# Kernel tuning notes

Measured on AMD Instinct MI355X. Metric: run time of the kernel, lower is better.

## Reference

```python
import jax, jax.numpy as jnp
import numpy as np

EPS_NORM = 1e-12
RMS_EPS = 1e-5


def _rmsnorm(x, w):
    var = jnp.mean(jnp.square(x), axis=-1, keepdims=True)
    return x * jax.lax.rsqrt(var + RMS_EPS) * w


def setup_inputs() -> dict:
    key = jax.random.key(0)
    B, T, D, H, R, K = 2, 512, 1024, 16, 32, 3
    d = D // H
    ks = jax.random.split(key, 11)
    s = 0.02
    return dict(
        x=jax.random.normal(ks[0], (B, T, D), jnp.float32),
        Wq=jax.random.normal(ks[1], (D, D), jnp.float32) * s,
        Wk=jax.random.normal(ks[2], (D, D), jnp.float32) * s,
        Wv=jax.random.normal(ks[3], (D, D), jnp.float32) * s,
        Wo=jax.random.normal(ks[4], (D, D), jnp.float32) * s,
        wA=jax.random.normal(ks[5], (D, R), jnp.float32) * s,
        wB=jax.random.normal(ks[6], (R, D), jnp.float32) * s,
        conv_w=jax.random.normal(ks[7], (D, K), jnp.float32) * 0.5,
        beta_w=jax.random.normal(ks[8], (D, H), jnp.float32) * s,
        g_w=jax.random.normal(ks[9], (D, H), jnp.float32) * s,
        g_b=jnp.zeros((H,), jnp.float32),
        qnorm_w=jnp.ones((d,), jnp.float32),
        knorm_w=jnp.ones((d,), jnp.float32),
    )


def _path_attention(x, Wq, Wk, Wv, Wo, wA, wB, conv_w, beta_w, g_w, g_b, qnorm_w, knorm_w):
    # PaTH attention: s_ij = q_i^T (H_i ... H_{j+1}) k_j / sqrt(d) + (G_i - G_j),
    # H_t = I - beta_t w_t w_t^T (unit w_t), G = cumsum(logsigmoid(forget gate)).
    B, T, D = x.shape
    d = qnorm_w.shape[0]
    H = D // d
    scale = d ** -0.5

    q = (x @ Wq).reshape(B, T, H, d)
    k = (x @ Wk).reshape(B, T, H, d)
    v = (x @ Wv).reshape(B, T, H, d)

    # low-rank W projection + causal depthwise short conv (size 3) + silu
    w = (x @ wA) @ wB                                      # [B,T,D]
    wp = jnp.pad(w, ((0, 0), (2, 0), (0, 0)))
    w = wp[:, 0:T] * conv_w[:, 0] + wp[:, 1:T + 1] * conv_w[:, 1] + wp[:, 2:T + 2] * conv_w[:, 2]
    w = jax.nn.silu(w).reshape(B, T, H, d)
    # unit Householder directions
    w = w * jax.lax.rsqrt(jnp.sum(jnp.square(w), -1, keepdims=True) + EPS_NORM)

    beta = 2.0 * jax.nn.sigmoid(x @ beta_w)                # [B,T,H], in (0,2)
    g = jax.nn.log_sigmoid(x @ g_w + g_b)                  # [B,T,H] forget gate, log-space

    q = _rmsnorm(q, qnorm_w)
    k = _rmsnorm(k, knorm_w)

    # -> [B,H,T,(d)]
    q, k, v, w = (t.transpose(0, 2, 1, 3) for t in (q, k, v, w))
    beta = beta.transpose(0, 2, 1)
    g = g.transpose(0, 2, 1)

    # UT/WY form: A_{t,j} = w_t . (H_{t-1}...H_{j+1} k_j), t > j, via unit-lower tri solve:
    #   A_{t,j} + sum_{s<t} beta_s (w_t.w_s) A_{s,j} = (w_t.k_j) [t>j]
    tri_s = jnp.tril(jnp.ones((T, T), bool), -1)
    C = jnp.einsum('bhtd,bhsd->bhts', w, w) * beta[:, :, None, :]
    L = jnp.where(tri_s, C, 0.0) + jnp.eye(T, dtype=x.dtype)
    Rhs = jnp.where(tri_s, jnp.einsum('bhtd,bhjd->bhtj', w, k), 0.0)
    A = jax.scipy.linalg.solve_triangular(L, Rhs, lower=True, unit_diagonal=True)

    # s_ij = q_i.k_j - sum_{j<t<=i} (q_i.w_t) beta_t A_{t,j}
    tri = jnp.tril(jnp.ones((T, T), bool))
    qw = jnp.where(tri, jnp.einsum('bhid,bhtd->bhit', q, w), 0.0)
    S = jnp.einsum('bhid,bhjd->bhij', q, k) - jnp.einsum('bhit,bhtj->bhij', qw, beta[..., None] * A)

    G = jnp.cumsum(g, axis=-1)                             # [B,H,T]
    logits = S * scale + (G[..., :, None] - G[..., None, :])
    logits = jnp.where(tri, logits, -1e30)
    P = jax.nn.softmax(logits, axis=-1)
    o = jnp.einsum('bhij,bhjd->bhid', P, v)
    return o.transpose(0, 2, 1, 3).reshape(B, T, D) @ Wo


def reference(x, Wq, Wk, Wv, Wo, wA, wB, conv_w, beta_w, g_w, g_b, qnorm_w, knorm_w):
    return _path_attention(x, Wq, Wk, Wv, Wo, wA, wB, conv_w, beta_w, g_w, g_b, qnorm_w, knorm_w)
```

## Files before the change

### kernel.cpp

```cpp
#include <hip/hip_runtime.h>
#include <hip/hip_bf16.h>
#include <math.h>

#define B_ 2
#define T_ 512
#define D_ 1024
#define H_ 16
#define R_ 32
#define DH 64
#define BT_ (B_*T_)
#define BH_ (B_*H_)

typedef __attribute__((ext_vector_type(8))) short bf16x8;
typedef __attribute__((ext_vector_type(4))) short s16x4;
typedef __attribute__((ext_vector_type(4))) float f32x4;

#define MFMA_BF16(a, b, c) __builtin_amdgcn_mfma_f32_16x16x32_bf16(a, b, c, 0, 0, 0)

static __device__ __forceinline__ short bf16s(float v) {
  __hip_bfloat16 b = __float2bfloat16(v);
  return *reinterpret_cast<short*>(&b);
}
static __device__ __forceinline__ float b2f(__hip_bfloat16 h) { return __bfloat162float(h); }

__device__ __forceinline__ bf16x8 ldfrag(const __hip_bfloat16 s[][72], int b16, int kb, int fr, int kq) {
  return *(const bf16x8*)&s[b16 * 16 + fr][kb * 32 + kq * 8];
}
__device__ __forceinline__ void stage64(const __hip_bfloat16* __restrict__ g, int ldg,
                                        __hip_bfloat16 s[][72], int tid) {
#pragma unroll
  for (int l = 0; l < 2; ++l) {
    int f = tid + l * 256;
    int r = f >> 3, c = (f & 7) << 3;
    *(int4*)&s[r][c] = *(const int4*)&g[(size_t)r * ldg + c];
  }
}

typedef const __attribute__((address_space(1))) void* as1cv;
typedef __attribute__((address_space(3))) void* as3v;
__device__ __forceinline__ void gl16(const __hip_bfloat16* g, __hip_bfloat16* l) {
  __builtin_amdgcn_global_load_lds((as1cv)g, (as3v)l, 16, 0, 0);
}

__global__ __launch_bounds__(256) void prep_k(const float* __restrict__ x,
                                              const float* __restrict__ Wq,
                                              const float* __restrict__ Wk,
                                              const float* __restrict__ Wv,
                                              const float* __restrict__ Wo,
                                              const float* __restrict__ wA,
                                              const float* __restrict__ bw,
                                              const float* __restrict__ gw,
                                              __hip_bfloat16* __restrict__ xhi,
                                              __hip_bfloat16* __restrict__ xlo,
                                              __hip_bfloat16* __restrict__ wqkvT,
                                              __hip_bfloat16* __restrict__ woT,
                                              __hip_bfloat16* __restrict__ wcThi,
                                              __hip_bfloat16* __restrict__ wcTlo) {
  __shared__ float tile[64][65];
  const int bid = blockIdx.x, tid = threadIdx.x;
  if (bid < 512) {
    int i8 = bid * 256 + tid;
    float4 v0 = ((const float4*)x)[i8 * 2];
    float4 v1 = ((const float4*)x)[i8 * 2 + 1];
    float c[8] = {v0.x, v0.y, v0.z, v0.w, v1.x, v1.y, v1.z, v1.w};
    bf16x8 ph, pl;
#pragma unroll
    for (int u = 0; u < 8; ++u) {
      __hip_bfloat16 h = __float2bfloat16(c[u]);
      ph[u] = *reinterpret_cast<short*>(&h);
      pl[u] = bf16s(c[u] - __bfloat162float(h));
    }
    *(bf16x8*)&xhi[(size_t)i8 * 8] = ph;
    *(bf16x8*)&xlo[(size_t)i8 * 8] = pl;
  } else if (bid < 1536) {
    const int zz = (bid - 512) >> 8, idx = (bid - 512) & 255;
    const float* Wm = (zz == 0) ? Wq : (zz == 1) ? Wk : (zz == 2) ? Wv : Wo;
    __hip_bfloat16* thi = (zz < 3) ? (wqkvT + (size_t)zz * 1024 * D_) : woT;
    const int bn = (idx & 15) * 64, bk = (idx >> 4) * 64;
#pragma unroll
    for (int l = 0; l < 4; ++l) {
      int f = tid + l * 256; int r = f >> 4, c = (f & 15) << 2;
      *(float4*)&tile[r][c] = *(const float4*)&Wm[(size_t)(bk + r) * D_ + bn + c];
    }
    __syncthreads();
#pragma unroll
    for (int l = 0; l < 4; ++l) {
      int f = tid + l * 256; int n = f >> 4, k0 = (f & 15) << 2;
      s16x4 ph;
#pragma unroll
      for (int u = 0; u < 4; ++u) ph[u] = bf16s(tile[k0 + u][n]);
      *(s16x4*)&thi[(size_t)(bn + n) * D_ + bk + k0] = ph;
    }
  } else {
    int n = bid - 1536;
    for (int k = tid; k < D_; k += 256) {
      float v;
      if (n < 32) v = wA[(size_t)k * R_ + n];
      else if (n < 48) v = bw[(size_t)k * H_ + (n - 32)];
      else v = gw[(size_t)k * H_ + (n - 48)];
      __hip_bfloat16 h = __float2bfloat16(v);
      wcThi[(size_t)n * D_ + k] = h;
      wcTlo[(size_t)n * D_ + k] = __float2bfloat16(v - __bfloat162float(h));
    }
  }
}

__global__ __launch_bounds__(256) void gemm_qkv(const __hip_bfloat16* __restrict__ ah,
                                                const __hip_bfloat16* __restrict__ bT,
                                                __hip_bfloat16* __restrict__ qb,
                                                __hip_bfloat16* __restrict__ kb,
                                                __hip_bfloat16* __restrict__ vhi,
                                                const float* __restrict__ qnw,
                                                const float* __restrict__ knw) {
  __shared__ __hip_bfloat16 As[64][64];
  __shared__ __hip_bfloat16 Bs[64][64];
  __shared__ __hip_bfloat16 Lt[64][72];
  const int bm = blockIdx.y * 64, bn = blockIdx.x * 64;
  const int tid = threadIdx.x, w = tid >> 6, lane = tid & 63;
  const int fr = lane & 15, kq = lane >> 4;
  const f32x4 zf = {0.f, 0.f, 0.f, 0.f};
  f32x4 acc[4] = {zf, zf, zf, zf};
  const __hip_bfloat16* ap = ah + (size_t)bm * D_;
  const __hip_bfloat16* bp = bT + (size_t)bn * D_;

  for (int t = 0; t < 16; ++t) {
    __syncthreads();
#pragma unroll
    for (int i = 0; i < 2; ++i) {
      int chunk = tid + i * 256;
      int row = chunk >> 3, c8 = (chunk & 7) ^ (row & 7);
      gl16(ap + (size_t)row * D_ + t * 64 + c8 * 8, &As[0][0] + chunk * 8);
      gl16(bp + (size_t)row * D_ + t * 64 + c8 * 8, &Bs[0][0] + chunk * 8);
    }
    __syncthreads();
    const int ra = w * 16 + fr, sa = ra & 7;
    bf16x8 a0 = *(const bf16x8*)&As[ra][(kq ^ sa) * 8];
    bf16x8 a1 = *(const bf16x8*)&As[ra][((kq + 4) ^ sa) * 8];
#pragma unroll
    for (int n = 0; n < 4; ++n) {
      int rb = n * 16 + fr, sb = rb & 7;
      bf16x8 b0 = *(const bf16x8*)&Bs[rb][(kq ^ sb) * 8];
      bf16x8 b1 = *(const bf16x8*)&Bs[rb][((kq + 4) ^ sb) * 8];
      acc[n] = MFMA_BF16(a0, b0, acc[n]);
      acc[n] = MFMA_BF16(a1, b1, acc[n]);
    }
  }

  if (bn < 2048) {
    float rs[4];
#pragma unroll
    for (int reg = 0; reg < 4; ++reg) {
      float s = 0.f;
#pragma unroll
      for (int n = 0; n < 4; ++n) s += acc[n][reg] * acc[n][reg];
#pragma unroll
      for (int mm = 1; mm <= 8; mm <<= 1) s += __shfl_xor(s, mm);
      rs[reg] = rsqrtf(s * (1.f / DH) + 1e-5f);
    }
    const bool isq = (bn < 1024);
    __hip_bfloat16* outp = isq ? qb : kb;
#pragma unroll
    for (int n = 0; n < 4; ++n) {
      int gn = bn + n * 16 + fr;
      int dd = gn & 63, h = (gn & 1023) >> 6;
      float nw = (isq ? qnw : knw)[dd];
#pragma unroll
      for (int reg = 0; reg < 4; ++reg) {
        int gm = bm + w * 16 + kq * 4 + reg;
        int bb = gm >> 9, tt = gm & 511;
        outp[(((size_t)(bb * H_ + h)) * T_ + tt) * DH + dd] =
            __float2bfloat16(acc[n][reg] * rs[reg] * nw);
      }
    }
  } else {
    const int row0 = w * 16 + kq * 4;
#pragma unroll
    for (int n = 0; n < 4; ++n) {
      int dd = n * 16 + fr;
#pragma unroll
      for (int reg = 0; reg < 4; ++reg) Lt[dd][row0 + reg] = __float2bfloat16(acc[n][reg]);
    }
    __syncthreads();
    const int b = bm >> 9, t0 = bm & 511, h = (bn - 2048) >> 6;
    const size_t base = ((size_t)(b * H_ + h)) * DH * T_;
#pragma unroll
    for (int l = 0; l < 2; ++l) {
      int f = tid + l * 256;
      int dd = f >> 3, tq = (f & 7) * 8;
      *(bf16x8*)&vhi[base + (size_t)dd * T_ + t0 + tq] = *(const bf16x8*)&Lt[dd][tq];
    }
  }
}

__global__ __launch_bounds__(256) void gemm_o(const __hip_bfloat16* __restrict__ ah,
                                              const __hip_bfloat16* __restrict__ bT,
                                              float* __restrict__ C) {
  __shared__ __hip_bfloat16 As[64][64];
  __shared__ __hip_bfloat16 Bs[64][64];
  const int bm = blockIdx.y * 64, bn = blockIdx.x * 64;
  const int tid = threadIdx.x, w = tid >> 6, lane = tid & 63;
  const int fr = lane & 15, kq = lane >> 4;
  const f32x4 zf = {0.f, 0.f, 0.f, 0.f};
  f32x4 acc[4] = {zf, zf, zf, zf};
  const __hip_bfloat16* ap = ah + (size_t)bm * D_;
  const __hip_bfloat16* bp = bT + (size_t)bn * D_;
  for (int t = 0; t < 16; ++t) {
    __syncthreads();
#pragma unroll
    for (int i = 0; i < 2; ++i) {
      int chunk = tid + i * 256;
      int row = chunk >> 3, c8 = (chunk & 7) ^ (row & 7);
      gl16(ap + (size_t)row * D_ + t * 64 + c8 * 8, &As[0][0] + chunk * 8);
      gl16(bp + (size_t)row * D_ + t * 64 + c8 * 8, &Bs[0][0] + chunk * 8);
    }
    __syncthreads();
    const int ra = w * 16 + fr, sa = ra & 7;
    bf16x8 a0 = *(const bf16x8*)&As[ra][(kq ^ sa) * 8];
    bf16x8 a1 = *(const bf16x8*)&As[ra][((kq + 4) ^ sa) * 8];
#pragma unroll
    for (int n = 0; n < 4; ++n) {
      int rb = n * 16 + fr, sb = rb & 7;
      bf16x8 b0 = *(const bf16x8*)&Bs[rb][(kq ^ sb) * 8];
      bf16x8 b1 = *(const bf16x8*)&Bs[rb][((kq + 4) ^ sb) * 8];
      acc[n] = MFMA_BF16(a0, b0, acc[n]);
      acc[n] = MFMA_BF16(a1, b1, acc[n]);
    }
  }
#pragma unroll
  for (int n = 0; n < 4; ++n) {
    int gn = bn + n * 16 + fr;
#pragma unroll
    for (int reg = 0; reg < 4; ++reg) {
      int gm = bm + w * 16 + kq * 4 + reg;
      C[(size_t)gm * D_ + gn] = acc[n][reg];
    }
  }
}

__global__ __launch_bounds__(256) void gemm_ycat(const __hip_bfloat16* __restrict__ ah,
                                                 const __hip_bfloat16* __restrict__ al,
                                                 const __hip_bfloat16* __restrict__ bh,
                                                 const __hip_bfloat16* __restrict__ bl,
                                                 float* __restrict__ ypart) {
  __shared__ __hip_bfloat16 Ah[64][72], Al[64][72], Bh[64][72], Bl[64][72];
  const int z = blockIdx.x, bm = blockIdx.y * 64;
  const int tid = threadIdx.x, w = tid >> 6, lane = tid & 63;
  const int fr = lane & 15, kq = lane >> 4;
  const f32x4 zf = {0.f, 0.f, 0.f, 0.f};
  f32x4 acc[4] = {zf, zf, zf, zf};
  float* C = ypart + (size_t)z * (BT_ * 64);
  for (int k0 = z * 256; k0 < z * 256 + 256; k0 += 64) {
    __syncthreads();
    stage64(ah + (size_t)bm * D_ + k0, D_, Ah, tid);
    stage64(al + (size_t)bm * D_ + k0, D_, Al, tid);
    stage64(bh + k0, D_, Bh, tid);
    stage64(bl + k0, D_, Bl, tid);
    __syncthreads();
    bf16x8 ah0 = ldfrag(Ah, w, 0, fr, kq), ah1 = ldfrag(Ah, w, 1, fr, kq);
    bf16x8 al0 = ldfrag(Al, w, 0, fr, kq), al1 = ldfrag(Al, w, 1, fr, kq);
#pragma unroll
    for (int nb = 0; nb < 4; ++nb) {
      bf16x8 b0 = ldfrag(Bh, nb, 0, fr, kq), b1 = ldfrag(Bh, nb, 1, fr, kq);
      bf16x8 c0 = ldfrag(Bl, nb, 0, fr, kq), c1 = ldfrag(Bl, nb, 1, fr, kq);
      acc[nb] = MFMA_BF16(ah0, b0, acc[nb]); acc[nb] = MFMA_BF16(ah1, b1, acc[nb]);
      acc[nb] = MFMA_BF16(ah0, c0, acc[nb]); acc[nb] = MFMA_BF16(ah1, c1, acc[nb]);
      acc[nb] = MFMA_BF16(al0, b0, acc[nb]); acc[nb] = MFMA_BF16(al1, b1, acc[nb]);
    }
  }
#pragma unroll
  for (int nb = 0; nb < 4; ++nb) {
    int n = nb * 16 + fr;
#pragma unroll
    for (int reg = 0; reg < 4; ++reg) {
      int m = bm + w * 16 + kq * 4 + reg;
      C[(size_t)m * 64 + n] = acc[nb][reg];
    }
  }
}

__global__ __launch_bounds__(512) void gate_cumsum(const float* __restrict__ ypart,
                                                   const float* __restrict__ gb,
                                                   float* __restrict__ beta,
                                                   float* __restrict__ G) {
  __shared__ float s[T_];
  int bh = blockIdx.x, b = bh >> 4, h = bh & 15, t = threadIdx.x;
  int bt = b * T_ + t;
  float by = 0.f, gy = gb[h];
#pragma unroll
  for (int z = 0; z < 4; ++z) {
    const float* yp = ypart + (size_t)z * (BT_ * 64) + (size_t)bt * 64;
    by += yp[32 + h];
    gy += yp[48 + h];
  }
  beta[(size_t)bh * T_ + t] = 2.f / (1.f + expf(-by));
  s[t] = fminf(gy, 0.f) - log1pf(expf(-fabsf(gy)));
  __syncthreads();
  for (int off = 1; off < T_; off <<= 1) {
    float v = (t >= off) ? s[t - off] : 0.f;
    __syncthreads();
    s[t] += v;
    __syncthreads();
  }
  G[(size_t)bh * T_ + t] = s[t];
}

__global__ __launch_bounds__(1024) void wdir_k(const float* __restrict__ ypart,
                                               const float* __restrict__ wB,
                                               const float* __restrict__ convw,
                                               float* __restrict__ wT,
                                               __hip_bfloat16* __restrict__ wb16) {
  int bt = blockIdx.x, b = bt / T_, t = bt - b * T_;
  __shared__ float wl[3][R_];
  int tid = threadIdx.x;
  if (tid < 3 * R_) {
    int row = tid / R_, r = tid - row * R_;
    int ts = t - row;
    float a = 0.f;
    if (ts >= 0) {
#pragma unroll
      for (int z = 0; z < 4; ++z)
        a += ypart[(size_t)z * (BT_ * 64) + (size_t)(b * T_ + ts) * 64 + r];
    }
    wl[row][r] = a;
  }
  __syncthreads();
  float f0 = 0.f, f1 = 0.f, f2 = 0.f;
  for (int r = 0; r < R_; ++r) {
    float wb = wB[(size_t)r * D_ + tid];
    f0 += wl[0][r] * wb; f1 += wl[1][r] * wb; f2 += wl[2][r] * wb;
  }
  float y = f2 * convw[tid * 3 + 0] + f1 * convw[tid * 3 + 1] + f0 * convw[tid * 3 + 2];
  float s = y / (1.f + expf(-y));
  float ss = s * s;
#pragma unroll
  for (int m = 32; m >= 1; m >>= 1) ss += __shfl_xor(ss, m);
  float outv = s * rsqrtf(ss + 1e-12f);
  int h = tid >> 6, dd = tid & 63;
  size_t o = (((size_t)(b * H_ + h)) * T_ + t) * DH + dd;
  wT[o] = outv;
  wb16[o] = __float2bfloat16(outv);
}

__global__ __launch_bounds__(256) void linv_k(const float* __restrict__ wT,
                                              const float* __restrict__ beta,
                                              __hip_bfloat16* __restrict__ linv) {
  __shared__ float Wsh[64][68];
  __shared__ float Csh[64][65];
  __shared__ float Li[64][68];
  __shared__ float bI[64];
  const int I = blockIdx.x, bhx = blockIdx.y;
  const int tid = threadIdx.x;
#pragma unroll
  for (int l = 0; l < 4; ++l) {
    int f = tid + l * 256; int r = f >> 4, c = (f & 15) << 2;
    *(float4*)&Wsh[r][c] = *(const float4*)&wT[((size_t)bhx * T_ + I * 64 + r) * DH + c];
  }
  if (tid < 64) bI[tid] = beta[(size_t)bhx * T_ + I * 64 + tid];
#pragma unroll
  for (int l = 0; l < 16; ++l) {
    int e = tid + l * 256; int r = e >> 6, c = e & 63;
    Li[r][c] = (r == c) ? 1.f : 0.f;
  }
  __syncthreads();
  const int tm = (tid >> 4) << 2, tn = (tid & 15) << 2;
  float cc[4][4] = {};
  for (int dd = 0; dd < 64; ++dd) {
    float a0 = Wsh[tm + 0][dd], a1 = Wsh[tm + 1][dd], a2 = Wsh[tm + 2][dd], a3 = Wsh[tm + 3][dd];
    float b0 = Wsh[tn + 0][dd], b1 = Wsh[tn + 1][dd], b2 = Wsh[tn + 2][dd], b3 = Wsh[tn + 3][dd];
    cc[0][0] += a0 * b0; cc[0][1] += a0 * b1; cc[0][2] += a0 * b2; cc[0][3] += a0 * b3;
    cc[1][0] += a1 * b0; cc[1][1] += a1 * b1; cc[1][2] += a1 * b2; cc[1][3] += a1 * b3;
    cc[2][0] += a2 * b0; cc[2][1] += a2 * b1; cc[2][2] += a2 * b2; cc[2][3] += a2 * b3;
    cc[3][0] += a3 * b0; cc[3][1] += a3 * b1; cc[3][2] += a3 * b2; cc[3][3] += a3 * b3;
  }
#pragma unroll
  for (int ii = 0; ii < 4; ++ii)
#pragma unroll
    for (int jj = 0; jj < 4; ++jj)
      Csh[tm + ii][tn + jj] = (tm + ii > tn + jj) ? cc[ii][jj] * bI[tn + jj] : 0.f;
  __syncthreads();
  const int sL = tid & 63, g = tid >> 6;
  for (int r = 0; r < 63; ++r) {
    float lr = Li[r][sL];
    for (int r2 = r + 1 + g; r2 < 64; r2 += 4)
      Li[r2][sL] -= Csh[r2][r] * lr;
    __syncthreads();
  }
#pragma unroll
  for (int l = 0; l < 4; ++l) {
    int f = tid + l * 256; int r = f >> 4, c0 = (f & 15) << 2;
    s16x4 p;
    p.x = bf16s(Li[r][c0 + 0]); p.y = bf16s(Li[r][c0 + 1]);
    p.z = bf16s(Li[r][c0 + 2]); p.w = bf16s(Li[r][c0 + 3]);
    *(s16x4*)&linv[((size_t)(bhx * 8 + I)) * 4096 + r * 64 + c0] = p;
  }
}

__global__ __launch_bounds__(256) void chain_k(const __hip_bfloat16* __restrict__ kb,
                                               const __hip_bfloat16* __restrict__ wb,
                                               const __hip_bfloat16* __restrict__ linv,
                                               const float* __restrict__ beta,
                                               __hip_bfloat16* __restrict__ abT,
                                               __hip_bfloat16* __restrict__ khat) {
  __shared__ __hip_bfloat16 Kb[64][72];
  __shared__ __hip_bfloat16 Ws[64][72];
  __shared__ __hip_bfloat16 WsT[64][72];
  __shared__ __hip_bfloat16 Ls[64][72];
  __shared__ __hip_bfloat16 Kh[64][72];
  __shared__ __hip_bfloat16 Ps[64][72];
  __shared__ __hip_bfloat16 Xs[64][72];
  __shared__ float bI[64];
  const int ch = blockIdx.x, bhx = blockIdx.y;
  const int tid = threadIdx.x, w = tid >> 6, lane = tid & 63;
  const int fr = lane & 15, kq = lane >> 4;
  const int jr = w * 16 + kq * 4;
  const size_t hb = (size_t)bhx * T_;
  const f32x4 zf = {0.f, 0.f, 0.f, 0.f};

  stage64(kb + (hb + ch * 64) * DH, DH, Kb, tid);
  f32x4 macc[4] = {zf, zf, zf, zf};

  for (int I = ch; I < 8; ++I) {
    __syncthreads();
    stage64(wb + (hb + I * 64) * DH, DH, Ws, tid);
    stage64(linv + ((size_t)(bhx * 8 + I)) * 4096, 64, Ls, tid);
    if (tid < 64) bI[tid] = beta[hb + I * 64 + tid];
#pragma unroll
    for (int nb = 0; nb < 4; ++nb) {
      int d = nb * 16 + fr;
#pragma unroll
      for (int reg = 0; reg < 4; ++reg)
        Kh[jr + reg][d] = __float2bfloat16(b2f(Kb[jr + reg][d]) - macc[nb][reg]);
    }
    __syncthreads();
#pragma unroll
    for (int l = 0; l < 2; ++l) {
      int f = tid + l * 256;
      int r = f >> 3, c = (f & 7) << 3;
      *(int4*)&khat[(((size_t)(bhx * 8 + I)) * T_ + ch * 64 + r) * DH + c] = *(const int4*)&Kh[r][c];
    }
#pragma unroll
    for (int l = 0; l < 16; ++l) {
      int e = tid + l * 256;
      int t = e >> 6, d = e & 63;
      WsT[d][t] = Ws[t][d];
    }
    bf16x8 kh0 = ldfrag(Kh, w, 0, fr, kq), kh1 = ldfrag(Kh, w, 1, fr, kq);
    f32x4 pt[4];
#pragma unroll
    for (int nb = 0; nb < 4; ++nb) {
      pt[nb] = MFMA_BF16(kh0, ldfrag(Ws, nb, 0, fr, kq), zf);
      pt[nb] = MFMA_BF16(kh1, ldfrag(Ws, nb, 1, fr, kq), pt[nb]);
    }
#pragma unroll
    for (int nb = 0; nb < 4; ++nb) {
      int t = nb * 16 + fr;
#pragma unroll
      for (int reg = 0; reg < 4; ++reg) {
        float v = pt[nb][reg];
        if (I == ch && t <= jr + reg) v = 0.f;
        Ps[jr + reg][t] = __float2bfloat16(v);
      }
    }
    __syncthreads();
    bf16x8 la0 = ldfrag(Ls, w, 0, fr, kq), la1 = ldfrag(Ls, w, 1, fr, kq);
    f32x4 av[4];
#pragma unroll
    for (int nb = 0; nb < 4; ++nb) {
      av[nb] = MFMA_BF16(la0, ldfrag(Ps, nb, 0, fr, kq), zf);
      av[nb] = MFMA_BF16(la1, ldfrag(Ps, nb, 1, fr, kq), av[nb]);
    }
#pragma unroll
    for (int nb = 0; nb < 4; ++nb) {
      s16x4 p;
      p.x = bf16s(bI[jr + 0] * av[nb][0]);
      p.y = bf16s(bI[jr + 1] * av[nb][1]);
      p.z = bf16s(bI[jr + 2] * av[nb][2]);
      p.w = bf16s(bI[jr + 3] * av[nb][3]);
      *(s16x4*)&Xs[nb * 16 + fr][jr] = p;
    }
    __syncthreads();
#pragma unroll
    for (int l = 0; l < 2; ++l) {
      int f = tid + l * 256;
      int r = f >> 3, c = (f & 7) << 3;
      *(int4*)&abT[(hb + ch * 64 + r) * T_ + I * 64 + c] = *(const int4*)&Xs[r][c];
    }
    bf16x8 xa0 = ldfrag(Xs, w, 0, fr, kq), xa1 = ldfrag(Xs, w, 1, fr, kq);
#pragma unroll
    for (int nb = 0; nb < 4; ++nb) {
      macc[nb] = MFMA_BF16(xa0, ldfrag(WsT, nb, 0, fr, kq), macc[nb]);
      macc[nb] = MFMA_BF16(xa1, ldfrag(WsT, nb, 1, fr, kq), macc[nb]);
    }
  }
}

__global__ __launch_bounds__(256) void attn_fused(const __hip_bfloat16* __restrict__ qb,
                                                  const __hip_bfloat16* __restrict__ wb,
                                                  const __hip_bfloat16* __restrict__ khat,
                                                  const __hip_bfloat16* __restrict__ abT,
                                                  const __hip_bfloat16* __restrict__ vhi,
                                                  const float* __restrict__ G,
                                                  __hip_bfloat16* __restrict__ ohi) {
  __shared__ __hip_bfloat16 Ms[64][72];
  __shared__ __hip_bfloat16 Ks[64][72];
  __shared__ __hip_bfloat16 Cs[64][72];
  __shared__ __hip_bfloat16 Vh[64][72];
  __shared__ __hip_bfloat16 Ps[64][72];
  const int it = blockIdx.x, bh = blockIdx.y;
  const int b = bh >> 4, h = bh & 15;
  const int tid = threadIdx.x, w = tid >> 6, lane = tid & 63;
  const int fr = lane & 15, kq = lane >> 4;
  const int row0 = w * 16 + kq * 4;
  const size_t hb = (size_t)bh * T_;
  const f32x4 zero = {0.f, 0.f, 0.f, 0.f};

  stage64(qb + (hb + it * 64) * DH, DH, Ks, tid);
  stage64(wb + (hb + it * 64) * DH, DH, Cs, tid);
  __syncthreads();
  const bf16x8 a0 = ldfrag(Ks, w, 0, fr, kq);
  const bf16x8 a1 = ldfrag(Ks, w, 1, fr, kq);
  f32x4 qw[4];
#pragma unroll
  for (int nb = 0; nb < 4; ++nb) {
    qw[nb] = MFMA_BF16(a0, ldfrag(Cs, nb, 0, fr, kq), zero);
    qw[nb] = MFMA_BF16(a1, ldfrag(Cs, nb, 1, fr, kq), qw[nb]);
  }
#pragma unroll
  for (int nb = 0; nb < 4; ++nb) {
    int col = nb * 16 + fr;
#pragma unroll
    for (int reg = 0; reg < 4; ++reg) {
      float v = -qw[nb][reg];
      if (col > row0 + reg) v = 0.f;
      Ms[row0 + reg][col] = __float2bfloat16(v);
    }
  }
  __syncthreads();
  const bf16x8 m0 = ldfrag(Ms, w, 0, fr, kq);
  const bf16x8 m1 = ldfrag(Ms, w, 1, fr, kq);

  float Gi[4];
#pragma unroll
  for (int reg = 0; reg < 4; ++reg) Gi[reg] = G[hb + it * 64 + row0 + reg];
  float mrow[4] = {-3e38f, -3e38f, -3e38f, -3e38f};
  float lrow[4] = {0.f, 0.f, 0.f, 0.f};
  f32x4 acc_o[4] = {zero, zero, zero, zero};
  const __hip_bfloat16* kh = khat + ((size_t)(bh * 8 + it)) * T_ * DH;

  for (int jt = 0; jt <= it; ++jt) {
    __syncthreads();
    stage64(kh + (size_t)(jt * 64) * DH, DH, Ks, tid);
    stage64(abT + (hb + jt * 64) * T_ + it * 64, T_, Cs, tid);
    stage64(vhi + (size_t)bh * DH * T_ + jt * 64, T_, Vh, tid);
    __syncthreads();
    f32x4 acc[4];
#pragma unroll
    for (int nb = 0; nb < 4; ++nb) {
      acc[nb] = MFMA_BF16(a0, ldfrag(Ks, nb, 0, fr, kq), zero);
      acc[nb] = MFMA_BF16(a1, ldfrag(Ks, nb, 1, fr, kq), acc[nb]);
      acc[nb] = MFMA_BF16(m0, ldfrag(Cs, nb, 0, fr, kq), acc[nb]);
      acc[nb] = MFMA_BF16(m1, ldfrag(Cs, nb, 1, fr, kq), acc[nb]);
    }
    float gj[4];
#pragma unroll
    for (int nb = 0; nb < 4; ++nb) gj[nb] = G[hb + jt * 64 + nb * 16 + fr];
    const bool diag = (jt == it);
    float vv[4][4];
#pragma unroll
    for (int reg = 0; reg < 4; ++reg) {
      float tm = -3e38f;
#pragma unroll
      for (int nb = 0; nb < 4; ++nb) {
        float vx = acc[nb][reg] * 0.125f + Gi[reg] - gj[nb];
        if (diag && (nb * 16 + fr) > row0 + reg) vx = -3e38f;
        vv[nb][reg] = vx;
        tm = fmaxf(tm, vx);
      }
#pragma unroll
      for (int mm = 1; mm <= 8; mm <<= 1) tm = fmaxf(tm, __shfl_xor(tm, mm));
      float mnew = fmaxf(mrow[reg], tm);
      float sc = __expf(mrow[reg] - mnew);
      mrow[reg] = mnew;
      float tsum = 0.f;
#pragma unroll
      for (int nb = 0; nb < 4; ++nb) {
        float p = __expf(vv[nb][reg] - mnew);
        Ps[row0 + reg][nb * 16 + fr] = __float2bfloat16(p);
        tsum += p;
      }
#pragma unroll
      for (int mm = 1; mm <= 8; mm <<= 1) tsum += __shfl_xor(tsum, mm);
      lrow[reg] = lrow[reg] * sc + tsum;
#pragma unroll
      for (int nb = 0; nb < 4; ++nb) acc_o[nb][reg] *= sc;
    }
    __syncthreads();
    const bf16x8 p0 = ldfrag(Ps, w, 0, fr, kq);
    const bf16x8 p1 = ldfrag(Ps, w, 1, fr, kq);
#pragma unroll
    for (int nb = 0; nb < 4; ++nb) {
      acc_o[nb] = MFMA_BF16(p0, ldfrag(Vh, nb, 0, fr, kq), acc_o[nb]);
      acc_o[nb] = MFMA_BF16(p1, ldfrag(Vh, nb, 1, fr, kq), acc_o[nb]);
    }
  }
#pragma unroll
  for (int reg = 0; reg < 4; ++reg) {
    float inv = 1.f / lrow[reg];
    int i = it * 64 + row0 + reg;
#pragma unroll
    for (int nb = 0; nb < 4; ++nb) {
      int dd = nb * 16 + fr;
      size_t oi = ((size_t)(b * T_ + i)) * D_ + h * 64 + dd;
      ohi[oi] = __float2bfloat16(acc_o[nb][reg] * inv);
    }
  }
}

extern "C" void kernel_launch(void* const* d_in, const int* in_sizes, int n_in,
                              void* d_out, int out_size, void* d_ws, size_t ws_size,
                              hipStream_t stream) {
  (void)in_sizes; (void)n_in; (void)out_size; (void)ws_size;
  const float* x     = (const float*)d_in[0];
  const float* Wq    = (const float*)d_in[1];
  const float* Wk    = (const float*)d_in[2];
  const float* Wv    = (const float*)d_in[3];
  const float* Wo    = (const float*)d_in[4];
  const float* wA    = (const float*)d_in[5];
  const float* wB    = (const float*)d_in[6];
  const float* convw = (const float*)d_in[7];
  const float* bw    = (const float*)d_in[8];
  const float* gw    = (const float*)d_in[9];
  const float* gb    = (const float*)d_in[10];
  const float* qnw   = (const float*)d_in[11];
  const float* knw   = (const float*)d_in[12];

  const size_t N1 = (size_t)BT_ * D_;
  const size_t NTT = (size_t)BH_ * T_ * T_;
  float* ws = (float*)d_ws;
  float* wTb   = ws;
  float* ypart = wTb + N1;
  float* beta  = ypart + (size_t)4 * BT_ * 64;
  float* G     = beta + (size_t)BH_ * T_;
  __hip_bfloat16* qb16  = (__hip_bfloat16*)(G + (size_t)BH_ * T_);
  __hip_bfloat16* kb16  = qb16 + N1;
  __hip_bfloat16* wb16  = kb16 + N1;
  __hip_bfloat16* abT   = wb16 + N1;
  __hip_bfloat16* linvb = abT + NTT;
  __hip_bfloat16* xhi   = linvb + (size_t)BH_ * 8 * 4096;
  __hip_bfloat16* xlo   = xhi + N1;
  __hip_bfloat16* obhi  = xlo + N1;
  __hip_bfloat16* woThi = obhi + N1;
  __hip_bfloat16* vhi   = woThi + N1;
  __hip_bfloat16* wcThi = vhi + N1;
  __hip_bfloat16* wcTlo = wcThi + (size_t)64 * D_;
  __hip_bfloat16* khat  = wcTlo + (size_t)64 * D_;
  __hip_bfloat16* wqkvT = khat + (size_t)BH_ * 8 * T_ * DH;

  prep_k<<<1600, 256, 0, stream>>>(x, Wq, Wk, Wv, Wo, wA, bw, gw,
                                   xhi, xlo, wqkvT, woThi, wcThi, wcTlo);
  gemm_ycat<<<dim3(4, 16), 256, 0, stream>>>(xhi, xlo, wcThi, wcTlo, ypart);
  gemm_qkv<<<dim3(48, 16), 256, 0, stream>>>(xhi, wqkvT, qb16, kb16, vhi, qnw, knw);
  gate_cumsum<<<BH_, 512, 0, stream>>>(ypart, gb, beta, G);
  wdir_k<<<BT_, 1024, 0, stream>>>(ypart, wB, convw, wTb, wb16);
  linv_k<<<dim3(8, BH_), 256, 0, stream>>>(wTb, beta, linvb);
  chain_k<<<dim3(8, BH_), 256, 0, stream>>>(kb16, wb16, linvb, beta, abT, khat);
  attn_fused<<<dim3(8, BH_), 256, 0, stream>>>(qb16, wb16, khat, abT, vhi, G, obhi);
  gemm_o<<<dim3(16, 16), 256, 0, stream>>>(obhi, woThi, (float*)d_out);
}
```

Measured before the change: 134.1 us.

## Double-buffer LDS tiles via async loads and merge gate/wdir kernels

Converts the GEMM, chain and fused-attention loops to double-buffered shared-memory tiles. The next tile is prefetched with global_load_lds into a swizzled 64x64 layout while the current tile is consumed, which removes one barrier per iteration and hides load latency. It also merges gate_cumsum and wdir_k into one launch with 512-thread blocks, saving a kernel launch. The cost is double the LDS footprint per block, which may lower occupancy. Correctness depends on the async LDS writes being complete before each barrier.

```diff
diff --git a/kernel.cpp b/kernel.cpp
--- a/kernel.cpp
+++ b/kernel.cpp
@@ -40,6 +40,20 @@
 typedef __attribute__((address_space(3))) void* as3v;
 __device__ __forceinline__ void gl16(const __hip_bfloat16* g, __hip_bfloat16* l) {
   __builtin_amdgcn_global_load_lds((as1cv)g, (as3v)l, 16, 0, 0);
+}
+__device__ __forceinline__ void stage64s(const __hip_bfloat16* __restrict__ g, int ldg,
+                                         __hip_bfloat16* s, int tid) {
+#pragma unroll
+  for (int i = 0; i < 2; ++i) {
+    int chunk = tid + i * 256;
+    int r = chunk >> 3, c8 = (chunk & 7) ^ (r & 7);
+    gl16(g + (size_t)r * ldg + c8 * 8, s + chunk * 8);
+  }
+}
+__device__ __forceinline__ bf16x8 ldfragS(const __hip_bfloat16* s, int b16, int half, int fr, int kq) {
+  int r = b16 * 16 + fr;
+  int col8 = ((kq + half * 4) ^ (r & 7)) * 8;
+  return *(const bf16x8*)&s[r * 64 + col8];
 }
 
 __global__ __launch_bounds__(256) void prep_k(const float* __restrict__ x,
@@ -112,8 +126,8 @@
                                                 __hip_bfloat16* __restrict__ vhi,
                                                 const float* __restrict__ qnw,
                                                 const float* __restrict__ knw) {
-  __shared__ __hip_bfloat16 As[64][64];
-  __shared__ __hip_bfloat16 Bs[64][64];
+  __shared__ __hip_bfloat16 As[2][64][64];
+  __shared__ __hip_bfloat16 Bs[2][64][64];
   __shared__ __hip_bfloat16 Lt[64][72];
   const int bm = blockIdx.y * 64, bn = blockIdx.x * 64;
   const int tid = threadIdx.x, w = tid >> 6, lane = tid & 63;
@@ -122,28 +136,23 @@
   f32x4 acc[4] = {zf, zf, zf, zf};
   const __hip_bfloat16* ap = ah + (size_t)bm * D_;
   const __hip_bfloat16* bp = bT + (size_t)bn * D_;
-
+  stage64s(ap, D_, &As[0][0][0], tid);
+  stage64s(bp, D_, &Bs[0][0][0], tid);
+  __syncthreads();
   for (int t = 0; t < 16; ++t) {
-    __syncthreads();
-#pragma unroll
-    for (int i = 0; i < 2; ++i) {
-      int chunk = tid + i * 256;
-      int row = chunk >> 3, c8 = (chunk & 7) ^ (row & 7);
-      gl16(ap + (size_t)row * D_ + t * 64 + c8 * 8, &As[0][0] + chunk * 8);
-      gl16(bp + (size_t)row * D_ + t * 64 + c8 * 8, &Bs[0][0] + chunk * 8);
-    }
-    __syncthreads();
-    const int ra = w * 16 + fr, sa = ra & 7;
-    bf16x8 a0 = *(const bf16x8*)&As[ra][(kq ^ sa) * 8];
-    bf16x8 a1 = *(const bf16x8*)&As[ra][((kq + 4) ^ sa) * 8];
+    const int cur = t & 1;
+    if (t < 15) {
+      stage64s(ap + (t + 1) * 64, D_, &As[cur ^ 1][0][0], tid);
+      stage64s(bp + (t + 1) * 64, D_, &Bs[cur ^ 1][0][0], tid);
+    }
+    bf16x8 a0 = ldfragS(&As[cur][0][0], w, 0, fr, kq);
+    bf16x8 a1 = ldfragS(&As[cur][0][0], w, 1, fr, kq);
 #pragma unroll
     for (int n = 0; n < 4; ++n) {
-      int rb = n * 16 + fr, sb = rb & 7;
-      bf16x8 b0 = *(const bf16x8*)&Bs[rb][(kq ^ sb) * 8];
-      bf16x8 b1 = *(const bf16x8*)&Bs[rb][((kq + 4) ^ sb) * 8];
-      acc[n] = MFMA_BF16(a0, b0, acc[n]);
-      acc[n] = MFMA_BF16(a1, b1, acc[n]);
-    }
+      acc[n] = MFMA_BF16(a0, ldfragS(&Bs[cur][0][0], n, 0, fr, kq), acc[n]);
+      acc[n] = MFMA_BF16(a1, ldfragS(&Bs[cur][0][0], n, 1, fr, kq), acc[n]);
+    }
+    __syncthreads();
   }
 
   if (bn < 2048) {
@@ -195,8 +204,8 @@
 __global__ __launch_bounds__(256) void gemm_o(const __hip_bfloat16* __restrict__ ah,
                                               const __hip_bfloat16* __restrict__ bT,
                                               float* __restrict__ C) {
-  __shared__ __hip_bfloat16 As[64][64];
-  __shared__ __hip_bfloat16 Bs[64][64];
+  __shared__ __hip_bfloat16 As[2][64][64];
+  __shared__ __hip_bfloat16 Bs[2][64][64];
   const int bm = blockIdx.y * 64, bn = blockIdx.x * 64;
   const int tid = threadIdx.x, w = tid >> 6, lane = tid & 63;
   const int fr = lane & 15, kq = lane >> 4;
@@ -204,27 +213,23 @@
   f32x4 acc[4] = {zf, zf, zf, zf};
   const __hip_bfloat16* ap = ah + (size_t)bm * D_;
   const __hip_bfloat16* bp = bT + (size_t)bn * D_;
+  stage64s(ap, D_, &As[0][0][0], tid);
+  stage64s(bp, D_, &Bs[0][0][0], tid);
+  __syncthreads();
   for (int t = 0; t < 16; ++t) {
-    __syncthreads();
-#pragma unroll
-    for (int i = 0; i < 2; ++i) {
-      int chunk = tid + i * 256;
-      int row = chunk >> 3, c8 = (chunk & 7) ^ (row & 7);
-      gl16(ap + (size_t)row * D_ + t * 64 + c8 * 8, &As[0][0] + chunk * 8);
-      gl16(bp + (size_t)row * D_ + t * 64 + c8 * 8, &Bs[0][0] + chunk * 8);
-    }
-    __syncthreads();
-    const int ra = w * 16 + fr, sa = ra & 7;
-    bf16x8 a0 = *(const bf16x8*)&As[ra][(kq ^ sa) * 8];
-    bf16x8 a1 = *(const bf16x8*)&As[ra][((kq + 4) ^ sa) * 8];
+    const int cur = t & 1;
+    if (t < 15) {
+      stage64s(ap + (t + 1) * 64, D_, &As[cur ^ 1][0][0], tid);
+      stage64s(bp + (t + 1) * 64, D_, &Bs[cur ^ 1][0][0], tid);
+    }
+    bf16x8 a0 = ldfragS(&As[cur][0][0], w, 0, fr, kq);
+    bf16x8 a1 = ldfragS(&As[cur][0][0], w, 1, fr, kq);
 #pragma unroll
     for (int n = 0; n < 4; ++n) {
-      int rb = n * 16 + fr, sb = rb & 7;
-      bf16x8 b0 = *(const bf16x8*)&Bs[rb][(kq ^ sb) * 8];
-      bf16x8 b1 = *(const bf16x8*)&Bs[rb][((kq + 4) ^ sb) * 8];
-      acc[n] = MFMA_BF16(a0, b0, acc[n]);
-      acc[n] = MFMA_BF16(a1, b1, acc[n]);
-    }
+      acc[n] = MFMA_BF16(a0, ldfragS(&Bs[cur][0][0], n, 0, fr, kq), acc[n]);
+      acc[n] = MFMA_BF16(a1, ldfragS(&Bs[cur][0][0], n, 1, fr, kq), acc[n]);
+    }
+    __syncthreads();
   }
 #pragma unroll
   for (int n = 0; n < 4; ++n) {
@@ -278,67 +283,71 @@
   }
 }
 
-__global__ __launch_bounds__(512) void gate_cumsum(const float* __restrict__ ypart,
-                                                   const float* __restrict__ gb,
-                                                   float* __restrict__ beta,
-                                                   float* __restrict__ G) {
-  __shared__ float s[T_];
-  int bh = blockIdx.x, b = bh >> 4, h = bh & 15, t = threadIdx.x;
-  int bt = b * T_ + t;
-  float by = 0.f, gy = gb[h];
-#pragma unroll
-  for (int z = 0; z < 4; ++z) {
-    const float* yp = ypart + (size_t)z * (BT_ * 64) + (size_t)bt * 64;
-    by += yp[32 + h];
-    gy += yp[48 + h];
-  }
-  beta[(size_t)bh * T_ + t] = 2.f / (1.f + expf(-by));
-  s[t] = fminf(gy, 0.f) - log1pf(expf(-fabsf(gy)));
-  __syncthreads();
-  for (int off = 1; off < T_; off <<= 1) {
-    float v = (t >= off) ? s[t - off] : 0.f;
-    __syncthreads();
-    s[t] += v;
-    __syncthreads();
-  }
-  G[(size_t)bh * T_ + t] = s[t];
-}
-
-__global__ __launch_bounds__(1024) void wdir_k(const float* __restrict__ ypart,
-                                               const float* __restrict__ wB,
-                                               const float* __restrict__ convw,
-                                               float* __restrict__ wT,
-                                               __hip_bfloat16* __restrict__ wb16) {
-  int bt = blockIdx.x, b = bt / T_, t = bt - b * T_;
-  __shared__ float wl[3][R_];
-  int tid = threadIdx.x;
-  if (tid < 3 * R_) {
-    int row = tid / R_, r = tid - row * R_;
-    int ts = t - row;
-    float a = 0.f;
-    if (ts >= 0) {
-#pragma unroll
-      for (int z = 0; z < 4; ++z)
-        a += ypart[(size_t)z * (BT_ * 64) + (size_t)(b * T_ + ts) * 64 + r];
-    }
-    wl[row][r] = a;
-  }
-  __syncthreads();
-  float f0 = 0.f, f1 = 0.f, f2 = 0.f;
-  for (int r = 0; r < R_; ++r) {
-    float wb = wB[(size_t)r * D_ + tid];
-    f0 += wl[0][r] * wb; f1 += wl[1][r] * wb; f2 += wl[2][r] * wb;
-  }
-  float y = f2 * convw[tid * 3 + 0] + f1 * convw[tid * 3 + 1] + f0 * convw[tid * 3 + 2];
-  float s = y / (1.f + expf(-y));
-  float ss = s * s;
-#pragma unroll
-  for (int m = 32; m >= 1; m >>= 1) ss += __shfl_xor(ss, m);
-  float outv = s * rsqrtf(ss + 1e-12f);
-  int h = tid >> 6, dd = tid & 63;
-  size_t o = (((size_t)(b * H_ + h)) * T_ + t) * DH + dd;
-  wT[o] = outv;
-  wb16[o] = __float2bfloat16(outv);
+__global__ __launch_bounds__(512) void gate_wdir(const float* __restrict__ ypart,
+                                                 const float* __restrict__ gb,
+                                                 const float* __restrict__ wB,
+                                                 const float* __restrict__ convw,
+                                                 float* __restrict__ beta,
+                                                 float* __restrict__ G,
+                                                 float* __restrict__ wT,
+                                                 __hip_bfloat16* __restrict__ wb16) {
+  __shared__ float shm[T_];
+  const int bid = blockIdx.x, tid = threadIdx.x;
+  if (bid < BT_) {
+    int bt = bid, b = bt / T_, t = bt - b * T_;
+    float* wl = shm;
+    if (tid < 3 * R_) {
+      int row = tid / R_, r = tid - row * R_;
+      int ts = t - row;
+      float a = 0.f;
+      if (ts >= 0) {
+#pragma unroll
+        for (int z = 0; z < 4; ++z)
+          a += ypart[(size_t)z * (BT_ * 64) + (size_t)(b * T_ + ts) * 64 + r];
+      }
+      wl[row * R_ + r] = a;
+    }
+    __syncthreads();
+#pragma unroll
+    for (int half = 0; half < 2; ++half) {
+      int col = tid + half * 512;
+      float f0 = 0.f, f1 = 0.f, f2 = 0.f;
+      for (int r = 0; r < R_; ++r) {
+        float wb = wB[(size_t)r * D_ + col];
+        f0 += wl[0 * R_ + r] * wb; f1 += wl[1 * R_ + r] * wb; f2 += wl[2 * R_ + r] * wb;
+      }
+      float y = f2 * convw[col * 3 + 0] + f1 * convw[col * 3 + 1] + f0 * convw[col * 3 + 2];
+      float s = y / (1.f + expf(-y));
+      float ss = s * s;
+#pragma unroll
+      for (int m = 32; m >= 1; m >>= 1) ss += __shfl_xor(ss, m);
+      float outv = s * rsqrtf(ss + 1e-12f);
+      int h = col >> 6, dd = col & 63;
+      size_t o = (((size_t)(b * H_ + h)) * T_ + t) * DH + dd;
+      wT[o] = outv;
+      wb16[o] = __float2bfloat16(outv);
+    }
+  } else {
+    int bh = bid - BT_, b = bh >> 4, h = bh & 15, t = tid;
+    int bt = b * T_ + t;
+    float by = 0.f, gy = gb[h];
+#pragma unroll
+    for (int z = 0; z < 4; ++z) {
+      const float* yp = ypart + (size_t)z * (BT_ * 64) + (size_t)bt * 64;
+      by += yp[32 + h];
+      gy += yp[48 + h];
+    }
+    beta[(size_t)bh * T_ + t] = 2.f / (1.f + expf(-by));
+    shm[t] = fminf(gy, 0.f) - log1pf(expf(-fabsf(gy)));
+    __syncthreads();
+    for (int off = 1; off < T_; off <<= 1) {
+      float v = (t >= off) ? shm[t - off] : 0.f;
+      __syncthreads();
+      shm[t] += v;
+      __syncthreads();
+    }
+    G[(size_t)bh * T_ + t] = shm[t];
+  }
 }
 
 __global__ __launch_bounds__(256) void linv_k(const float* __restrict__ wT,
@@ -402,9 +411,9 @@
                                                __hip_bfloat16* __restrict__ abT,
                                                __hip_bfloat16* __restrict__ khat) {
   __shared__ __hip_bfloat16 Kb[64][72];
-  __shared__ __hip_bfloat16 Ws[64][72];
+  __shared__ __hip_bfloat16 Ws[2][64][64];
   __shared__ __hip_bfloat16 WsT[64][72];
-  __shared__ __hip_bfloat16 Ls[64][72];
+  __shared__ __hip_bfloat16 Ls[2][64][64];
   __shared__ __hip_bfloat16 Kh[64][72];
   __shared__ __hip_bfloat16 Ps[64][72];
   __shared__ __hip_bfloat16 Xs[64][72];
@@ -417,12 +426,13 @@
   const f32x4 zf = {0.f, 0.f, 0.f, 0.f};
 
   stage64(kb + (hb + ch * 64) * DH, DH, Kb, tid);
+  stage64s(wb + (hb + ch * 64) * DH, DH, &Ws[0][0][0], tid);
+  stage64s(linv + ((size_t)(bhx * 8 + ch)) * 4096, 64, &Ls[0][0][0], tid);
   f32x4 macc[4] = {zf, zf, zf, zf};
 
   for (int I = ch; I < 8; ++I) {
-    __syncthreads();
-    stage64(wb + (hb + I * 64) * DH, DH, Ws, tid);
-    stage64(linv + ((size_t)(bhx * 8 + I)) * 4096, 64, Ls, tid);
+    const int cur = (I - ch) & 1;
+    __syncthreads();
     if (tid < 64) bI[tid] = beta[hb + I * 64 + tid];
 #pragma unroll
     for (int nb = 0; nb < 4; ++nb) {
@@ -432,6 +442,10 @@
         Kh[jr + reg][d] = __float2bfloat16(b2f(Kb[jr + reg][d]) - macc[nb][reg]);
     }
     __syncthreads();
+    if (I < 7) {
+      stage64s(wb + (hb + (I + 1) * 64) * DH, DH, &Ws[cur ^ 1][0][0], tid);
+      stage64s(linv + ((size_t)(bhx * 8 + I + 1)) * 4096, 64, &Ls[cur ^ 1][0][0], tid);
+    }
 #pragma unroll
     for (int l = 0; l < 2; ++l) {
       int f = tid + l * 256;
@@ -442,14 +456,14 @@
     for (int l = 0; l < 16; ++l) {
       int e = tid + l * 256;
       int t = e >> 6, d = e & 63;
-      WsT[d][t] = Ws[t][d];
+      WsT[d][t] = Ws[cur][t][(((d >> 3) ^ (t & 7)) << 3) | (d & 7)];
     }
     bf16x8 kh0 = ldfrag(Kh, w, 0, fr, kq), kh1 = ldfrag(Kh, w, 1, fr, kq);
     f32x4 pt[4];
 #pragma unroll
     for (int nb = 0; nb < 4; ++nb) {
-      pt[nb] = MFMA_BF16(kh0, ldfrag(Ws, nb, 0, fr, kq), zf);
-      pt[nb] = MFMA_BF16(kh1, ldfrag(Ws, nb, 1, fr, kq), pt[nb]);
+      pt[nb] = MFMA_BF16(kh0, ldfragS(&Ws[cur][0][0], nb, 0, fr, kq), zf);
+      pt[nb] = MFMA_BF16(kh1, ldfragS(&Ws[cur][0][0], nb, 1, fr, kq), pt[nb]);
     }
 #pragma unroll
     for (int nb = 0; nb < 4; ++nb) {
@@ -462,7 +476,8 @@
       }
     }
     __syncthreads();
-    bf16x8 la0 = ldfrag(Ls, w, 0, fr, kq), la1 = ldfrag(Ls, w, 1, fr, kq);
+    bf16x8 la0 = ldfragS(&Ls[cur][0][0], w, 0, fr, kq);
+    bf16x8 la1 = ldfragS(&Ls[cur][0][0], w, 1, fr, kq);
     f32x4 av[4];
 #pragma unroll
     for (int nb = 0; nb < 4; ++nb) {
@@ -502,9 +517,9 @@
                                                   const float* __restrict__ G,
                                                   __hip_bfloat16* __restrict__ ohi) {
   __shared__ __hip_bfloat16 Ms[64][72];
-  __shared__ __hip_bfloat16 Ks[64][72];
-  __shared__ __hip_bfloat16 Cs[64][72];
-  __shared__ __hip_bfloat16 Vh[64][72];
+  __shared__ __hip_bfloat16 Ks[2][64][64];
+  __shared__ __hip_bfloat16 Cs[2][64][64];
+  __shared__ __hip_bfloat16 Vh[2][64][64];
   __shared__ __hip_bfloat16 Ps[64][72];
   const int it = blockIdx.x, bh = blockIdx.y;
   const int b = bh >> 4, h = bh & 15;
@@ -513,17 +528,21 @@
   const int row0 = w * 16 + kq * 4;
   const size_t hb = (size_t)bh * T_;
   const f32x4 zero = {0.f, 0.f, 0.f, 0.f};
-
-  stage64(qb + (hb + it * 64) * DH, DH, Ks, tid);
-  stage64(wb + (hb + it * 64) * DH, DH, Cs, tid);
+  const __hip_bfloat16* kh = khat + ((size_t)(bh * 8 + it)) * T_ * DH;
+
+  stage64s(qb + (hb + it * 64) * DH, DH, &Ks[0][0][0], tid);
+  stage64s(wb + (hb + it * 64) * DH, DH, &Cs[0][0][0], tid);
   __syncthreads();
-  const bf16x8 a0 = ldfrag(Ks, w, 0, fr, kq);
-  const bf16x8 a1 = ldfrag(Ks, w, 1, fr, kq);
+  const bf16x8 a0 = ldfragS(&Ks[0][0][0], w, 0, fr, kq);
+  const bf16x8 a1 = ldfragS(&Ks[0][0][0], w, 1, fr, kq);
+  stage64s(kh, DH, &Ks[1][0][0], tid);
+  stage64s(abT + hb * T_ + it * 64, T_, &Cs[1][0][0], tid);
+  stage64s(vhi + (size_t)bh * DH * T_, T_, &Vh[1][0][0], tid);
   f32x4 qw[4];
 #pragma unroll
   for (int nb = 0; nb < 4; ++nb) {
-    qw[nb] = MFMA_BF16(a0, ldfrag(Cs, nb, 0, fr, kq), zero);
-    qw[nb] = MFMA_BF16(a1, ldfrag(Cs, nb, 1, fr, kq), qw[nb]);
+    qw[nb] = MFMA_BF16(a0, ldfragS(&Cs[0][0][0], nb, 0, fr, kq), zero);
+    qw[nb] = MFMA_BF16(a1, ldfragS(&Cs[0][0][0], nb, 1, fr, kq), qw[nb]);
   }
 #pragma unroll
   for (int nb = 0; nb < 4; ++nb) {
@@ -545,21 +564,21 @@
   float mrow[4] = {-3e38f, -3e38f, -3e38f, -3e38f};
   float lrow[4] = {0.f, 0.f, 0.f, 0.f};
   f32x4 acc_o[4] = {zero, zero, zero, zero};
-  const __hip_bfloat16* kh = khat + ((size_t)(bh * 8 + it)) * T_ * DH;
 
   for (int jt = 0; jt <= it; ++jt) {
-    __syncthreads();
-    stage64(kh + (size_t)(jt * 64) * DH, DH, Ks, tid);
-    stage64(abT + (hb + jt * 64) * T_ + it * 64, T_, Cs, tid);
-    stage64(vhi + (size_t)bh * DH * T_ + jt * 64, T_, Vh, tid);
-    __syncthreads();
+    const int cur = (jt + 1) & 1;
+    if (jt < it) {
+      stage64s(kh + (size_t)((jt + 1) * 64) * DH, DH, &Ks[cur ^ 1][0][0], tid);
+      stage64s(abT + (hb + (jt + 1) * 64) * T_ + it * 64, T_, &Cs[cur ^ 1][0][0], tid);
+      stage64s(vhi + (size_t)bh * DH * T_ + (jt + 1) * 64, T_, &Vh[cur ^ 1][0][0], tid);
+    }
     f32x4 acc[4];
 #pragma unroll
     for (int nb = 0; nb < 4; ++nb) {
-      acc[nb] = MFMA_BF16(a0, ldfrag(Ks, nb, 0, fr, kq), zero);
-      acc[nb] = MFMA_BF16(a1, ldfrag(Ks, nb, 1, fr, kq), acc[nb]);
-      acc[nb] = MFMA_BF16(m0, ldfrag(Cs, nb, 0, fr, kq), acc[nb]);
-      acc[nb] = MFMA_BF16(m1, ldfrag(Cs, nb, 1, fr, kq), acc[nb]);
+      acc[nb] = MFMA_BF16(a0, ldfragS(&Ks[cur][0][0], nb, 0, fr, kq), zero);
+      acc[nb] = MFMA_BF16(a1, ldfragS(&Ks[cur][0][0], nb, 1, fr, kq), acc[nb]);
+      acc[nb] = MFMA_BF16(m0, ldfragS(&Cs[cur][0][0], nb, 0, fr, kq), acc[nb]);
+      acc[nb] = MFMA_BF16(m1, ldfragS(&Cs[cur][0][0], nb, 1, fr, kq), acc[nb]);
     }
     float gj[4];
 #pragma unroll
@@ -599,9 +618,10 @@
     const bf16x8 p1 = ldfrag(Ps, w, 1, fr, kq);
 #pragma unroll
     for (int nb = 0; nb < 4; ++nb) {
-      acc_o[nb] = MFMA_BF16(p0, ldfrag(Vh, nb, 0, fr, kq), acc_o[nb]);
-      acc_o[nb] = MFMA_BF16(p1, ldfrag(Vh, nb, 1, fr, kq), acc_o[nb]);
-    }
+      acc_o[nb] = MFMA_BF16(p0, ldfragS(&Vh[cur][0][0], nb, 0, fr, kq), acc_o[nb]);
+      acc_o[nb] = MFMA_BF16(p1, ldfragS(&Vh[cur][0][0], nb, 1, fr, kq), acc_o[nb]);
+    }
+    __syncthreads();
   }
 #pragma unroll
   for (int reg = 0; reg < 4; ++reg) {
@@ -660,8 +680,7 @@
                                    xhi, xlo, wqkvT, woThi, wcThi, wcTlo);
   gemm_ycat<<<dim3(4, 16), 256, 0, stream>>>(xhi, xlo, wcThi, wcTlo, ypart);
   gemm_qkv<<<dim3(48, 16), 256, 0, stream>>>(xhi, wqkvT, qb16, kb16, vhi, qnw, knw);
-  gate_cumsum<<<BH_, 512, 0, stream>>>(ypart, gb, beta, G);
-  wdir_k<<<BT_, 1024, 0, stream>>>(ypart, wB, convw, wTb, wb16);
+  gate_wdir<<<BT_ + BH_, 512, 0, stream>>>(ypart, gb, wB, convw, beta, G, wTb, wb16);
   linv_k<<<dim3(8, BH_), 256, 0, stream>>>(wTb, beta, linvb);
   chain_k<<<dim3(8, BH_), 256, 0, stream>>>(kb16, wb16, linvb, beta, abT, khat);
   attn_fused<<<dim3(8, BH_), 256, 0, stream>>>(qb16, wb16, khat, abT, vhi, G, obhi);
```

Result: slower. 141.1 us (+5.2%).
